# Optimization experiments

Hardware: AMD Instinct MI355X
Metric: run time of the kernel (lower is better)

Reference implementation:

```python
import jax, jax.numpy as jnp
import numpy as np

B, C, H, W = 2, 256, 64, 64
HEADS, SR = 8, 4
D = C // HEADS          # head dim = 32
N = H * W               # query length = 4096
EPS = 1e-5


def _conv(x, w, stride=1, pad=0, groups=1, b=None):
    out = jax.lax.conv_general_dilated(
        x, w, (stride, stride), [(pad, pad), (pad, pad)],
        dimension_numbers=('NCHW', 'OIHW', 'NCHW'),
        feature_group_count=groups)
    if b is not None:
        out = out + b[None, :, None, None]
    return out


def _bn(x, p):
    # p: [4, C] = (gamma, beta, running_mean, running_var), eval-mode BN
    g, b, m, v = p[0], p[1], p[2], p[3]
    s = g / jnp.sqrt(v + EPS)
    return (x - m[None, :, None, None]) * s[None, :, None, None] + b[None, :, None, None]


def setup_inputs() -> dict:
    key = jax.random.key(0)
    ks = iter(jax.random.split(key, 32))
    nrm = lambda shape, s=0.05: jax.random.normal(next(ks), shape, jnp.float32) * s
    def bnp():
        return jnp.stack([jnp.ones((C,), jnp.float32), jnp.zeros((C,), jnp.float32),
                          jax.random.normal(next(ks), (C,), jnp.float32) * 0.1,
                          jax.random.uniform(next(ks), (C,), jnp.float32) + 0.5])
    return dict(
        x=jax.random.normal(next(ks), (B, C, H, W), jnp.float32),
        relative_pos_enc=jax.random.normal(next(ks), (B, 2, 64, 64), jnp.float32),
        q_w=nrm((C, C, 1, 1)), q_b=jnp.zeros((C,), jnp.float32),
        kv_w=nrm((2 * C, C, 1, 1)), kv_b=jnp.zeros((2 * C,), jnp.float32),
        sr1_dw_w=nrm((C, 1, SR + 3, SR + 3)), sr1_bn1=bnp(),
        sr1_pw_w=nrm((C, 1, 1, 1), 0.5), sr1_bn2=bnp(),
        sr2_dw_w=nrm((C, 1, SR // 2 + 3, SR // 2 + 3)), sr2_bn1=bnp(),
        sr2_pw_w=nrm((C, 1, 1, 1), 0.5), sr2_bn2=bnp(),
        local_w=nrm((C, 1, 3, 3)), local_b=jnp.zeros((C,), jnp.float32),
    )


def reference(x, relative_pos_enc, q_w, q_b, kv_w, kv_b,
              sr1_dw_w, sr1_bn1, sr1_pw_w, sr1_bn2,
              sr2_dw_w, sr2_bn1, sr2_pw_w, sr2_bn2,
              local_w, local_b):
    scale = D ** -0.5
    # q: 1x1 conv -> [B, heads, N, D]; both branches use the FIRST half of heads
    q = _conv(x, q_w, b=q_b).reshape(B, HEADS, D, N).transpose(0, 1, 3, 2)
    qh = q[:, :HEADS // 2]

    def branch(dw_w, bn1, pw_w, bn2, stride, pad, rpe_slice):
        # SR path: depthwise conv + BN + ReLU, depthwise 1x1 + BN
        y = jax.nn.relu(_bn(_conv(x, dw_w, stride, pad, groups=C), bn1))
        y = _bn(_conv(y, pw_w, groups=C), bn2)
        # local 3x3 depthwise mixing with residual
        y = _conv(y, local_w, pad=1, groups=C, b=local_b) + y
        kv = _conv(y, kv_w, b=kv_b)                # [B, 2C, h', w']
        k, v = jnp.split(kv, 2, axis=1)
        L = 2 * y.shape[2] * y.shape[3]            # channel-fold doubles kv length
        k = k.reshape(B, HEADS // 2, D, L)
        v = v.reshape(B, HEADS // 2, D, L).transpose(0, 1, 3, 2)
        attn = jnp.einsum('bhnd,bhdl->bhnl', qh, k) * scale
        rpe = jax.image.resize(rpe_slice, (B, 1, N, L), method='bicubic')
        attn = jax.nn.softmax(attn + rpe, axis=-1)
        return jnp.einsum('bhnl,bhld->bhnd', attn, v)

    x1 = branch(sr1_dw_w, sr1_bn1, sr1_pw_w, sr1_bn2,
                SR, (SR + 3) // 2, relative_pos_enc[:, 0:1])
    x2 = branch(sr2_dw_w, sr2_bn1, sr2_pw_w, sr2_bn2,
                SR // 2, (SR // 2 + 3) // 2, relative_pos_enc[:, 1:2])
    out = jnp.concatenate([x1, x2], axis=-1)       # [B, heads//2, N, 2D]
    return out.reshape(B, C, H, W)
```

## Files before the change

### kernel.cpp

```cpp
#include <hip/hip_runtime.h>
#include <hip/hip_bf16.h>
#include <math.h>

#define NB 2
#define NC 256
#define HWIN 4096
#define NN 4096
#define ND 32
#define NHH 4
#define EPSV 1e-5f

typedef short short8 __attribute__((ext_vector_type(8)));
typedef float f32x4 __attribute__((ext_vector_type(4)));
typedef unsigned short u16;
typedef unsigned int u32;

#define OFF_T1   0
#define OFF_T2   262144
#define OFF_Q    1310720
#define OFF_KT1  1835008
#define OFF_VT1  1900544
#define OFF_KT2  1966080
#define OFF_VT2  2228224
#define OFF_RCT1 2490368
#define OFF_RCT2 2531328
#define OFF_WT   2695168
#define OFF_PO   2826240
#define OFF_PS   4923392
#define OFF_QWT  5054464

#define QSCALE 0.2550437314857726f
#define LOG2E  1.4426950408889634f

__device__ __forceinline__ u16 f2bf(float x) {
  unsigned u = __float_as_uint(x);
  u += 0x7fffu + ((u >> 16) & 1u);
  return (u16)(u >> 16);
}

__device__ __forceinline__ u32 pk_bf16(float a, float b) {
  __hip_bfloat162 h = __float22bfloat162_rn(make_float2(a, b));
  u32 r; __builtin_memcpy(&r, &h, 4);
  return r;
}

__device__ __forceinline__ float keysw(float t) {
  t = fabsf(t);
  float w;
  if (t < 1.f)       w = ((1.5f*t - 2.5f)*t)*t + 1.f;
  else if (t < 2.f)  w = ((-0.5f*t + 2.5f)*t - 4.f)*t + 2.f;
  else               w = 0.f;
  return w;
}

template<int KS, int STR, int PAD, int OH>
__device__ __forceinline__ void dwconv_body(int idx, const float* __restrict__ x,
    const float* __restrict__ dww, const float* __restrict__ bn1,
    const float* __restrict__ pww, const float* __restrict__ bn2,
    float* __restrict__ tout) {
  const int hw = OH*OH;
  int s = idx % hw; int c = (idx/hw) % NC; int b = idx/(hw*NC);
  int oy = s / OH, ox = s % OH;
  const float* xp = x + (b*NC + c)*HWIN;
  const float* wp = dww + c*KS*KS;
  float acc = 0.f;
  #pragma unroll
  for (int ky = 0; ky < KS; ++ky) {
    int iy = oy*STR - PAD + ky;
    if (iy < 0 || iy >= 64) continue;
    #pragma unroll
    for (int kx = 0; kx < KS; ++kx) {
      int ix = ox*STR - PAD + kx;
      if (ix < 0 || ix >= 64) continue;
      acc += xp[iy*64 + ix] * wp[ky*KS + kx];
    }
  }
  float s1 = bn1[c] * rsqrtf(bn1[3*NC + c] + EPSV);
  float z = (acc - bn1[2*NC + c])*s1 + bn1[NC + c];
  z = fmaxf(z, 0.f);
  float s2 = bn2[c] * rsqrtf(bn2[3*NC + c] + EPSV);
  z = z * (pww[c]*s2) + (bn2[NC + c] - bn2[2*NC + c]*s2);
  tout[idx] = z;
}

__device__ __forceinline__ void rpe_body(int idx, const float* __restrict__ rpe,
                                         u16* __restrict__ rcT, int L, int ch) {
  int r = idx & 63; int l = (idx >> 6) % L; int b = idx / (64*L);
  float f = ((float)l + 0.5f)*(64.f/(float)L) - 0.5f;
  int i0 = (int)floorf(f) - 1;
  const float* rp = rpe + ((b*2 + ch)*64 + r)*64;
  float v = 0.f, wsum = 0.f;
  #pragma unroll
  for (int j = 0; j < 4; ++j) {
    int i = i0 + j;
    if (i >= 0 && i < 64) {
      float w = keysw(f - (float)i);
      v += w * rp[i]; wsum += w;
    }
  }
  rcT[((size_t)(b*L + l))*80 + 4 + r] = f2bf(v / wsum);
}

__global__ void __launch_bounds__(256) prep_kernel(
    const float* __restrict__ x,
    const float* __restrict__ dw1, const float* __restrict__ bn11,
    const float* __restrict__ pw1, const float* __restrict__ bn12, float* __restrict__ t1,
    const float* __restrict__ dw2, const float* __restrict__ bn21,
    const float* __restrict__ pw2, const float* __restrict__ bn22, float* __restrict__ t2,
    const float* __restrict__ rpe, u16* __restrict__ rct1, u16* __restrict__ rct2,
    const float* __restrict__ kvw, float* __restrict__ wtp,
    const float* __restrict__ qw, float* __restrict__ qwtp) {
  int blk = blockIdx.x;
  int t = threadIdx.x;
  if (blk < 512) {
    dwconv_body<7,4,3,16>(blk*256 + t, x, dw1, bn11, pw1, bn12, t1);
  } else if (blk < 2560) {
    dwconv_body<5,2,2,32>((blk-512)*256 + t, x, dw2, bn21, pw2, bn22, t2);
  } else if (blk < 2816) {
    rpe_body((blk-2560)*256 + t, rpe, rct1, 512, 0);
  } else if (blk < 3840) {
    rpe_body((blk-2816)*256 + t, rpe, rct2, 2048, 1);
  } else if (blk < 3968) {
    int idx = (blk-3840)*256 + t;
    float4 vv = *(const float4*)(kvw + (size_t)idx*4);
    int o = idx >> 6, c4 = idx & 63;
    *(float4*)(wtp + ((size_t)(c4*512 + o))*4) = vv;
  } else {
    int idx = (blk-3968)*256 + t;
    float4 vv = *(const float4*)(qw + (size_t)idx*4);
    int oc = idx >> 6, c4 = idx & 63;
    *(float4*)(qwtp + ((size_t)(c4*128 + oc))*4) = vv;
  }
}

__global__ void __launch_bounds__(256) localkv_kernel(
    const float* __restrict__ t1in, const float* __restrict__ t2in,
    const float* __restrict__ lw, const float* __restrict__ lb,
    const float* __restrict__ wtp, const float* __restrict__ kvb,
    u16* __restrict__ kt1, u16* __restrict__ vt1,
    u16* __restrict__ kt2, u16* __restrict__ vt2,
    const float* __restrict__ x, const float* __restrict__ qwtp,
    const float* __restrict__ qb, u16* __restrict__ q) {
  __shared__ float sbuf[NC*8];
  int blk = blockIdx.x, tid = threadIdx.x;
  if (blk < 640) {
    int si = blk >> 1, kv = blk & 1;
    const float* tin; u16 *kT, *vT; int OH, hw, b, s0;
    if (si < 64) { tin = t1in; kT = kt1; vT = vt1; OH = 16; hw = 256;  b = si >> 5;  s0 = (si & 31)*8; }
    else { int v = si-64; tin = t2in; kT = kt2; vT = vt2; OH = 32; hw = 1024; b = v >> 7; s0 = (v & 127)*8; }
    int oy = s0 / OH, ox0 = s0 % OH;
    int ci = tid >> 3, i = tid & 7;
    int ox = ox0 + i;
    #pragma unroll
    for (int p = 0; p < 8; ++p) {
      int c = p*32 + ci;
      const float* tp = tin + (b*NC + c)*hw;
      const float* wp = lw + c*9;
      float acc = lb[c];
      #pragma unroll
      for (int dy = 0; dy < 3; ++dy) {
        int iy = oy + dy - 1;
        if (iy < 0 || iy >= OH) continue;
        #pragma unroll
        for (int dx = 0; dx < 3; ++dx) {
          int ix = ox + dx - 1;
          if (ix < 0 || ix >= OH) continue;
          acc += tp[iy*OH + ix]*wp[dy*3 + dx];
        }
      }
      acc += tp[oy*OH + ox];
      sbuf[c*8 + i] = acc;
    }
    __syncthreads();
    float acc[8];
    float bias = kvb[tid + kv*256];
    #pragma unroll
    for (int j = 0; j < 8; ++j) acc[j] = bias;
    const float* wrow = wtp + (size_t)(tid + kv*256)*4;
    #pragma unroll 4
    for (int c4 = 0; c4 < 64; ++c4) {
      f32x4 w4 = *(const f32x4*)(wrow + (size_t)c4*2048);
      #pragma unroll
      for (int j = 0; j < 4; ++j) {
        int c = c4*4 + j;
        f32x4 ya = *(const f32x4*)(sbuf + c*8);
        f32x4 yb = *(const f32x4*)(sbuf + c*8 + 4);
        float wv = w4[j];
        #pragma unroll
        for (int jj = 0; jj < 4; ++jj) { acc[jj] += wv*ya[jj]; acc[4+jj] += wv*yb[jj]; }
      }
    }
    int hh2 = tid >> 6, r = tid & 63, d = r >> 1, e = r & 1;
    int L = 2*hw;
    if (kv == 0) {
      u16* kp = kT + ((size_t)((b*NHH + hh2)*L + e*hw + s0))*ND + d;
      #pragma unroll
      for (int j = 0; j < 8; ++j) kp[j*ND] = f2bf(acc[j]);
    } else {
      int l0v = e*hw + s0;
      u16* vp = vT + ((size_t)((b*NHH + hh2)*(L/64) + (l0v >> 6))*ND + d)*64 + (l0v & 63);
      #pragma unroll
      for (int j = 0; j < 8; ++j) vp[j] = f2bf(acc[j]);
    }
  } else {
    int blk2 = blk - 640;
    int b = blk2 >> 9;
    int n0 = (blk2 & 511) * 8;
    #pragma unroll
    for (int j = 0; j < 8; ++j) {
      int idx = tid + 256*j;
      int c = idx >> 3, i = idx & 7;
      sbuf[idx] = x[(b*NC + c)*HWIN + n0 + i];
    }
    __syncthreads();
    int sph = tid >> 7, oc = tid & 127;
    float bias = qb[oc];
    float acc[4];
    #pragma unroll
    for (int i = 0; i < 4; ++i) acc[i] = bias;
    const float* wrow = qwtp + (size_t)oc*4;
    #pragma unroll 4
    for (int c4 = 0; c4 < 64; ++c4) {
      f32x4 w4 = *(const f32x4*)(wrow + (size_t)c4*512);
      #pragma unroll
      for (int j = 0; j < 4; ++j) {
        int c = c4*4 + j;
        f32x4 yv = *(const f32x4*)(sbuf + c*8 + sph*4);
        float wv = w4[j];
        #pragma unroll
        for (int i = 0; i < 4; ++i) acc[i] += wv * yv[i];
      }
    }
    int h = oc >> 5, d = oc & 31;
    u16* qp = q + (((size_t)(b*NHH + h))*NN + n0 + sph*4)*ND + d;
    #pragma unroll
    for (int i = 0; i < 4; ++i) qp[i*ND] = f2bf(acc[i]*QSCALE);
  }
}

__global__ void __launch_bounds__(256) attn_kernel(
    const u16* __restrict__ qbf,
    const u16* __restrict__ kt1, const u16* __restrict__ vt1, const u16* __restrict__ rct1,
    const u16* __restrict__ kt2, const u16* __restrict__ vt2, const u16* __restrict__ rct2,
    u32* __restrict__ po32, float* __restrict__ ps,
    float* __restrict__ out) {
  __shared__ u16 kbuf[64*32];
  __shared__ u16 vbuf[32*64];
  __shared__ u32 pbuf_all[4][16*32];
  int u = blockIdx.x;
  int br, b, hh, rb, chunk;
  if (u < 512) { br = 0; b = u >> 8; hh = (u >> 6) & 3; rb = u & 63; chunk = 0; }
  else { int v = u - 512; br = 1; chunk = v & 3; rb = (v >> 2) & 63; hh = (v >> 8) & 3; b = v >> 10; }
  int L = br ? 2048 : 512;
  const u16* kT  = br ? kt2 : kt1;
  const u16* vT  = br ? vt2 : vt1;
  const u16* rcT = br ? rct2 : rct1;
  int l0base = chunk * 512;
  int tid = threadIdx.x;
  int w = tid >> 6, lane = tid & 63;
  int g = lane >> 4, lo = lane & 15;
  u32* pbuf = pbuf_all[w];
  u16* pbuf16 = (u16*)pbuf;
  int n = rb*64 + w*16 + lo;

  const u16* kbase = kT + (size_t)(b*NHH + hh)*L*ND;
  const u16* vbase = vT + (size_t)(b*NHH + hh)*ND*L;
  const u16* rcTb  = rcT + (size_t)b*L*80;

  short8 qf = *(const short8*)(qbf + (((size_t)(b*NHH + hh))*NN + n)*ND + 8*g);

  float fr = ((float)n + 0.5f)*(1.f/64.f) - 0.5f;
  int ri0 = (int)floorf(fr) - 1;
  int a = (w < 2) ? rb - 2 : rb - 1;
  int rmin = a & ~3;
  float wr4[4]; float wsum = 0.f;
  #pragma unroll
  for (int j = 0; j < 4; ++j) {
    int i = ri0 + j;
    float wv = (i >= 0 && i < 64) ? keysw(fr - (float)i) : 0.f;
    wr4[j] = wv; wsum += wv;
  }
  float invw = LOG2E / wsum;
  float wt8[8];
  #pragma unroll
  for (int s = 0; s < 8; ++s) {
    float acc = 0.f;
    #pragma unroll
    for (int j = 0; j < 4; ++j)
      acc += (ri0 + j - rmin == s) ? wr4[j]*invw : 0.f;
    wt8[s] = acc;
  }
  short8 wtf;
  {
    u32 p0 = pk_bf16(wt8[0], wt8[1]), p1 = pk_bf16(wt8[2], wt8[3]);
    u32 p2 = pk_bf16(wt8[4], wt8[5]), p3 = pk_bf16(wt8[6], wt8[7]);
    uint4 uu = make_uint4(p0, p1, p2, p3);
    wtf = __builtin_bit_cast(short8, uu);
    if (g != 0) wtf = (short8)0;
  }
  const u16* rcrow0 = rcTb + (rmin + 4);

  const f32x4 zero = {0.f, 0.f, 0.f, 0.f};
  float ssum = 0.f;
  f32x4 o0 = zero, o1 = zero;

  int kr_row = tid >> 2, kr_col = (tid & 3)*8;
  int kr_sw  = ((kr_row >> 1) & 3)*8;
  int vr_row = tid >> 3, vr_col = (tid & 7)*8;
  int vr_sw  = (vr_row & 7)*8;
  int ksw = ((lo >> 1) & 3)*8;
  int vsw = (lo & 7)*8;
  int psw4 = (lo & 7)*4;
  int psw8 = (lo & 7)*8;

  auto stageLoad = [&](short8& kr, short8& vr, int l0) {
    kr = *(const short8*)(kbase + (size_t)(l0 + kr_row)*ND + kr_col);
    vr = *(const short8*)(vbase + (size_t)(l0 >> 6)*(ND*64) + vr_row*64 + vr_col);
  };
  auto stageStore = [&](short8 kr, short8 vr) {
    *(short8*)(kbuf + kr_row*32 + (kr_col ^ kr_sw)) = kr;
    *(short8*)(vbuf + vr_row*64 + (vr_col ^ vr_sw)) = vr;
  };
  auto loadRC = [&](uint4 (&rc)[4], int l0) {
    #pragma unroll
    for (int c = 0; c < 4; ++c) {
      const u16* arow = rcrow0 + (size_t)(l0 + 16*c + lo)*80;
      uint2 ra = *(const uint2*)arow;
      uint2 rb2 = *(const uint2*)(arow + 4);
      rc[c] = make_uint4(ra.x, ra.y, rb2.x, rb2.y);
    }
  };

  short8 kr, vr;
  uint4 rcA[4], rcB[4];
  stageLoad(kr, vr, l0base);
  loadRC(rcA, l0base);

  for (int t = 0; t < 8; ++t) {
    stageStore(kr, vr);
    __syncthreads();
    if (t < 7) { stageLoad(kr, vr, l0base + (t+1)*64); loadRC(rcB, l0base + (t+1)*64); }
    f32x4 s4[4];
    #pragma unroll
    for (int c = 0; c < 4; ++c) {
      short8 rcf = __builtin_bit_cast(short8, rcA[c]);
      f32x4 accr = __builtin_amdgcn_mfma_f32_16x16x32_bf16(rcf, wtf, zero, 0, 0, 0);
      short8 kf = *(const short8*)(kbuf + (16*c + lo)*32 + ((8*g) ^ ksw));
      s4[c] = __builtin_amdgcn_mfma_f32_16x16x32_bf16(kf, qf, accr, 0, 0, 0);
    }
    float psum = 0.f;
    u32 pk[8];
    #pragma unroll
    for (int c = 0; c < 4; ++c) {
      float p0 = __builtin_amdgcn_exp2f(s4[c][0]);
      float p1 = __builtin_amdgcn_exp2f(s4[c][1]);
      float p2 = __builtin_amdgcn_exp2f(s4[c][2]);
      float p3 = __builtin_amdgcn_exp2f(s4[c][3]);
      psum += (p0 + p1) + (p2 + p3);
      pk[2*c]   = pk_bf16(p0, p1);
      pk[2*c+1] = pk_bf16(p2, p3);
    }
    ssum += psum;
    #pragma unroll
    for (int c = 0; c < 4; ++c)
      *(uint2*)(pbuf + lo*32 + ((8*c + 2*g) ^ psw4)) = make_uint2(pk[2*c], pk[2*c+1]);
    short8 pf0 = *(const short8*)(pbuf16 + lo*64 + ((8*g) ^ psw8));
    short8 pf1 = *(const short8*)(pbuf16 + lo*64 + ((32 + 8*g) ^ psw8));
    short8 v00 = *(const short8*)(vbuf + lo*64 + ((8*g) ^ vsw));
    short8 v01 = *(const short8*)(vbuf + lo*64 + ((32 + 8*g) ^ vsw));
    short8 v10 = *(const short8*)(vbuf + (16 + lo)*64 + ((8*g) ^ vsw));
    short8 v11 = *(const short8*)(vbuf + (16 + lo)*64 + ((32 + 8*g) ^ vsw));
    o0 = __builtin_amdgcn_mfma_f32_16x16x32_bf16(v00, pf0, o0, 0, 0, 0);
    o1 = __builtin_amdgcn_mfma_f32_16x16x32_bf16(v10, pf0, o1, 0, 0, 0);
    o0 = __builtin_amdgcn_mfma_f32_16x16x32_bf16(v01, pf1, o0, 0, 0, 0);
    o1 = __builtin_amdgcn_mfma_f32_16x16x32_bf16(v11, pf1, o1, 0, 0, 0);
    if (t < 7) {
      #pragma unroll
      for (int j = 0; j < 4; ++j) rcA[j] = rcB[j];
    }
    __syncthreads();
  }

  ssum += __shfl_xor(ssum, 16, 64);
  ssum += __shfl_xor(ssum, 32, 64);
  if (br == 0) {
    float inv = 1.f/ssum;
    f32x4 w0 = o0*inv, w1 = o1*inv;
    float* op = out + ((size_t)((b*NC + hh*64 + rb)*64 + (w*16 + lo)))*64;
    *(f32x4*)(op + 4*g)      = w0;
    *(f32x4*)(op + 16 + 4*g) = w1;
  } else {
    int bh = b*NHH + hh;
    int row = bh*NN + n;
    u32* pop = po32 + ((size_t)chunk*32768 + row)*16;
    pop[2*g]     = pk_bf16(o0[0], o0[1]);
    pop[2*g + 1] = pk_bf16(o0[2], o0[3]);
    pop[8 + 2*g]     = pk_bf16(o1[0], o1[1]);
    pop[8 + 2*g + 1] = pk_bf16(o1[2], o1[3]);
    if (g == 0) ps[(size_t)chunk*32768 + row] = ssum;
  }
}

__global__ void __launch_bounds__(256) combine_kernel(
    const u32* __restrict__ po32, const float* __restrict__ ps,
    float* __restrict__ out) {
  int gid = blockIdx.x*256 + threadIdx.x;
  int row = gid >> 2, part = gid & 3;
  float sden = ps[row] + ps[32768 + row] + ps[65536 + row] + ps[98304 + row];
  float inv = 1.f/sden;
  float o[8];
  #pragma unroll
  for (int i = 0; i < 8; ++i) o[i] = 0.f;
  #pragma unroll
  for (int chunk = 0; chunk < 4; ++chunk) {
    const u32* pp = po32 + ((size_t)chunk*32768 + row)*16 + part*4;
    uint4 a = *(const uint4*)pp;
    u32 av[4] = {a.x, a.y, a.z, a.w};
    #pragma unroll
    for (int j = 0; j < 4; ++j) {
      o[2*j]   += __uint_as_float(av[j] << 16);
      o[2*j+1] += __uint_as_float(av[j] & 0xffff0000u);
    }
  }
  int bh = row >> 12, n = row & 4095;
  float* op = out + ((size_t)(((bh>>2)*NC + (bh&3)*64 + (n>>6))*64 + (n&63)))*64 + 32 + part*8;
  #pragma unroll
  for (int j = 0; j < 2; ++j) {
    f32x4 v = {o[4*j]*inv, o[4*j+1]*inv, o[4*j+2]*inv, o[4*j+3]*inv};
    *(f32x4*)(op + 4*j) = v;
  }
}

extern "C" void kernel_launch(void* const* d_in, const int* in_sizes, int n_in,
                              void* d_out, int out_size, void* d_ws, size_t ws_size,
                              hipStream_t stream) {
  const float* x    = (const float*)d_in[0];
  const float* rpe  = (const float*)d_in[1];
  const float* qw   = (const float*)d_in[2];
  const float* qb   = (const float*)d_in[3];
  const float* kvw  = (const float*)d_in[4];
  const float* kvb  = (const float*)d_in[5];
  const float* dw1  = (const float*)d_in[6];
  const float* bn11 = (const float*)d_in[7];
  const float* pw1  = (const float*)d_in[8];
  const float* bn12 = (const float*)d_in[9];
  const float* dw2  = (const float*)d_in[10];
  const float* bn21 = (const float*)d_in[11];
  const float* pw2  = (const float*)d_in[12];
  const float* bn22 = (const float*)d_in[13];
  const float* lw   = (const float*)d_in[14];
  const float* lb   = (const float*)d_in[15];
  float* out = (float*)d_out;
  float* ws  = (float*)d_ws;

  float* t1   = ws + OFF_T1;
  float* t2   = ws + OFF_T2;
  u16*   q    = (u16*)(ws + OFF_Q);
  u16*   kt1  = (u16*)(ws + OFF_KT1);
  u16*   vt1  = (u16*)(ws + OFF_VT1);
  u16*   kt2  = (u16*)(ws + OFF_KT2);
  u16*   vt2  = (u16*)(ws + OFF_VT2);
  u16*   rct1 = (u16*)(ws + OFF_RCT1);
  u16*   rct2 = (u16*)(ws + OFF_RCT2);
  float* wtp  = ws + OFF_WT;
  u32*   po32 = (u32*)(ws + OFF_PO);
  float* ps   = ws + OFF_PS;
  float* qwtp = ws + OFF_QWT;

  hipLaunchKernelGGL(prep_kernel, dim3(4000), dim3(256), 0, stream,
                     x, dw1, bn11, pw1, bn12, t1, dw2, bn21, pw2, bn22, t2,
                     rpe, rct1, rct2, kvw, wtp, qw, qwtp);
  hipLaunchKernelGGL(localkv_kernel, dim3(1664), dim3(256), 0, stream,
                     t1, t2, lw, lb, wtp, kvb, kt1, vt1, kt2, vt2, x, qwtp, qb, q);
  hipLaunchKernelGGL(attn_kernel, dim3(2560), dim3(256), 0, stream,
                     q, kt1, vt1, rct1, kt2, vt2, rct2, po32, ps, out);
  hipLaunchKernelGGL(combine_kernel, dim3(512), dim3(256), 0, stream,
                     po32, ps, out);
}
```

Measured before the change: 177.9 us.

## Retile localkv kernel to 128-thread blocks, one block computing both K and V

The local-mixing and KV projection part now gives each 128-thread block 4 spatial positions. Each thread computes 4 output channels covering both K and V, instead of splitting K and V across two blocks that each recompute the local 3x3 conv. This removes the duplicated depthwise conv work. The Q projection branch drops its shared-memory staging and reads x directly from global memory as float4 per channel, with 4 positions per block. Grid and block sizes change to match. The trade-off is more blocks, uncached direct global reads of x in the Q path, and higher register use per thread from the 16 accumulators.

```diff
diff --git a/kernel.cpp b/kernel.cpp
--- a/kernel.cpp
+++ b/kernel.cpp
@@ -133,7 +133,7 @@
   }
 }
 
-__global__ void __launch_bounds__(256) localkv_kernel(
+__global__ void __launch_bounds__(128) localkv_kernel(
     const float* __restrict__ t1in, const float* __restrict__ t2in,
     const float* __restrict__ lw, const float* __restrict__ lb,
     const float* __restrict__ wtp, const float* __restrict__ kvb,
@@ -141,15 +141,14 @@
     u16* __restrict__ kt2, u16* __restrict__ vt2,
     const float* __restrict__ x, const float* __restrict__ qwtp,
     const float* __restrict__ qb, u16* __restrict__ q) {
-  __shared__ float sbuf[NC*8];
+  __shared__ float sbuf[NC*4];
   int blk = blockIdx.x, tid = threadIdx.x;
   if (blk < 640) {
-    int si = blk >> 1, kv = blk & 1;
     const float* tin; u16 *kT, *vT; int OH, hw, b, s0;
-    if (si < 64) { tin = t1in; kT = kt1; vT = vt1; OH = 16; hw = 256;  b = si >> 5;  s0 = (si & 31)*8; }
-    else { int v = si-64; tin = t2in; kT = kt2; vT = vt2; OH = 32; hw = 1024; b = v >> 7; s0 = (v & 127)*8; }
+    if (blk < 128) { tin = t1in; kT = kt1; vT = vt1; OH = 16; hw = 256;  b = blk >> 6;  s0 = (blk & 63)*4; }
+    else { int v = blk-128; tin = t2in; kT = kt2; vT = vt2; OH = 32; hw = 1024; b = v >> 8; s0 = (v & 255)*4; }
     int oy = s0 / OH, ox0 = s0 % OH;
-    int ci = tid >> 3, i = tid & 7;
+    int ci = tid >> 2, i = tid & 3;
     int ox = ox0 + i;
     #pragma unroll
     for (int p = 0; p < 8; ++p) {
@@ -169,70 +168,74 @@
         }
       }
       acc += tp[oy*OH + ox];
-      sbuf[c*8 + i] = acc;
+      sbuf[c*4 + i] = acc;
     }
     __syncthreads();
-    float acc[8];
-    float bias = kvb[tid + kv*256];
-    #pragma unroll
-    for (int j = 0; j < 8; ++j) acc[j] = bias;
-    const float* wrow = wtp + (size_t)(tid + kv*256)*4;
-    #pragma unroll 4
+    float acc[4][4];
+    #pragma unroll
+    for (int k = 0; k < 4; ++k) {
+      float bias = kvb[tid + k*128];
+      #pragma unroll
+      for (int j = 0; j < 4; ++j) acc[k][j] = bias;
+    }
+    #pragma unroll 2
     for (int c4 = 0; c4 < 64; ++c4) {
-      f32x4 w4 = *(const f32x4*)(wrow + (size_t)c4*2048);
+      f32x4 w0 = *(const f32x4*)(wtp + ((size_t)(c4*512 + tid))*4);
+      f32x4 w1 = *(const f32x4*)(wtp + ((size_t)(c4*512 + tid + 128))*4);
+      f32x4 w2 = *(const f32x4*)(wtp + ((size_t)(c4*512 + tid + 256))*4);
+      f32x4 w3 = *(const f32x4*)(wtp + ((size_t)(c4*512 + tid + 384))*4);
       #pragma unroll
       for (int j = 0; j < 4; ++j) {
-        int c = c4*4 + j;
-        f32x4 ya = *(const f32x4*)(sbuf + c*8);
-        f32x4 yb = *(const f32x4*)(sbuf + c*8 + 4);
-        float wv = w4[j];
+        f32x4 y = *(const f32x4*)(sbuf + (c4*4 + j)*4);
         #pragma unroll
-        for (int jj = 0; jj < 4; ++jj) { acc[jj] += wv*ya[jj]; acc[4+jj] += wv*yb[jj]; }
+        for (int jj = 0; jj < 4; ++jj) {
+          acc[0][jj] += w0[j]*y[jj];
+          acc[1][jj] += w1[j]*y[jj];
+          acc[2][jj] += w2[j]*y[jj];
+          acc[3][jj] += w3[j]*y[jj];
+        }
       }
     }
-    int hh2 = tid >> 6, r = tid & 63, d = r >> 1, e = r & 1;
     int L = 2*hw;
-    if (kv == 0) {
-      u16* kp = kT + ((size_t)((b*NHH + hh2)*L + e*hw + s0))*ND + d;
-      #pragma unroll
-      for (int j = 0; j < 8; ++j) kp[j*ND] = f2bf(acc[j]);
-    } else {
-      int l0v = e*hw + s0;
-      u16* vp = vT + ((size_t)((b*NHH + hh2)*(L/64) + (l0v >> 6))*ND + d)*64 + (l0v & 63);
-      #pragma unroll
-      for (int j = 0; j < 8; ++j) vp[j] = f2bf(acc[j]);
+    #pragma unroll
+    for (int k = 0; k < 4; ++k) {
+      int o = tid + k*128;
+      if (k < 2) {
+        int hh2 = o >> 6, e = o & 1, d = (o & 63) >> 1;
+        u16* kp = kT + ((size_t)((b*NHH + hh2)*L + e*hw + s0))*ND + d;
+        #pragma unroll
+        for (int j = 0; j < 4; ++j) kp[j*ND] = f2bf(acc[k][j]);
+      } else {
+        int ov = o - 256;
+        int hh2 = ov >> 6, e = ov & 1, d = (ov & 63) >> 1;
+        int l0v = e*hw + s0;
+        u16* vp = vT + ((size_t)((b*NHH + hh2)*(L/64) + (l0v >> 6))*ND + d)*64 + (l0v & 63);
+        #pragma unroll
+        for (int j = 0; j < 4; ++j) vp[j] = f2bf(acc[k][j]);
+      }
     }
   } else {
-    int blk2 = blk - 640;
-    int b = blk2 >> 9;
-    int n0 = (blk2 & 511) * 8;
-    #pragma unroll
-    for (int j = 0; j < 8; ++j) {
-      int idx = tid + 256*j;
-      int c = idx >> 3, i = idx & 7;
-      sbuf[idx] = x[(b*NC + c)*HWIN + n0 + i];
-    }
-    __syncthreads();
-    int sph = tid >> 7, oc = tid & 127;
+    int qblk = blk - 640;
+    int b = qblk >> 10;
+    int n0 = (qblk & 1023) * 4;
+    int oc = tid;
     float bias = qb[oc];
     float acc[4];
     #pragma unroll
     for (int i = 0; i < 4; ++i) acc[i] = bias;
-    const float* wrow = qwtp + (size_t)oc*4;
-    #pragma unroll 4
+    const float* xb = x + (size_t)b*NC*HWIN + n0;
+    #pragma unroll 2
     for (int c4 = 0; c4 < 64; ++c4) {
-      f32x4 w4 = *(const f32x4*)(wrow + (size_t)c4*512);
+      f32x4 w4 = *(const f32x4*)(qwtp + ((size_t)(c4*128 + oc))*4);
       #pragma unroll
       for (int j = 0; j < 4; ++j) {
-        int c = c4*4 + j;
-        f32x4 yv = *(const f32x4*)(sbuf + c*8 + sph*4);
-        float wv = w4[j];
+        f32x4 xv = *(const f32x4*)(xb + (size_t)(c4*4 + j)*HWIN);
         #pragma unroll
-        for (int i = 0; i < 4; ++i) acc[i] += wv * yv[i];
+        for (int i = 0; i < 4; ++i) acc[i] += w4[j] * xv[i];
       }
     }
     int h = oc >> 5, d = oc & 31;
-    u16* qp = q + (((size_t)(b*NHH + h))*NN + n0 + sph*4)*ND + d;
+    u16* qp = q + (((size_t)(b*NHH + h))*NN + n0)*ND + d;
     #pragma unroll
     for (int i = 0; i < 4; ++i) qp[i*ND] = f2bf(acc[i]*QSCALE);
   }
@@ -470,7 +473,7 @@
   hipLaunchKernelGGL(prep_kernel, dim3(4000), dim3(256), 0, stream,
                      x, dw1, bn11, pw1, bn12, t1, dw2, bn21, pw2, bn22, t2,
                      rpe, rct1, rct2, kvw, wtp, qw, qwtp);
-  hipLaunchKernelGGL(localkv_kernel, dim3(1664), dim3(256), 0, stream,
+  hipLaunchKernelGGL(localkv_kernel, dim3(2688), dim3(128), 0, stream,
                      t1, t2, lw, lb, wtp, kvb, kt1, vt1, kt2, vt2, x, qwtp, qb, q);
   hipLaunchKernelGGL(attn_kernel, dim3(2560), dim3(256), 0, stream,
                      q, kt1, vt1, rct1, kt2, vt2, rct2, po32, ps, out);
```

Measured after the change: 180.2 us. About the same (+1.3%).
